# Optimization experiments

Hardware: AMD Instinct MI355X
Metric: run time of the kernel (lower is better)

Reference implementation:

```python
import jax, jax.numpy as jnp
import numpy as np

N = 50000
E = 500000
HID = 64
HEADS = 4
LAYERS = 4
CDIM = 8


def _p(key, shape, scale=0.05):
    return jax.random.normal(key, shape, dtype=jnp.float32) * scale


def setup_inputs() -> dict:
    key = jax.random.key(0)
    ks = jax.random.split(key, 32)
    x = jax.random.normal(ks[0], (N, 8), dtype=jnp.float32)
    src = jax.random.randint(ks[1], (E,), 0, N)
    dst = jax.random.randint(ks[2], (E,), 0, N)
    edge_index = jnp.stack([src, dst]).astype(jnp.int64)
    HC = HEADS * HID
    inp = {
        "x": x,
        "edge_index": edge_index,
        # encoder: Linear(8,64), ELU, Linear(64,64), ELU
        "enc_w1": _p(ks[3], (HID, 8)), "enc_b1": _p(ks[4], (HID,)),
        "enc_w2": _p(ks[5], (HID, HID)), "enc_b2": _p(ks[6], (HID,)),
        # per-layer TransformerConv params, stacked over layers
        "Wq": _p(ks[7], (LAYERS, HC, HID)), "bq": _p(ks[8], (LAYERS, HC)),
        "Wk": _p(ks[9], (LAYERS, HC, HID)), "bk": _p(ks[10], (LAYERS, HC)),
        "Wv": _p(ks[11], (LAYERS, HC, HID)), "bv": _p(ks[12], (LAYERS, HC)),
        "Ws": _p(ks[13], (LAYERS, HID, HID)), "bs": _p(ks[14], (LAYERS, HID)),
        # output MLP: 64->64->32->8
        "out_w1": _p(ks[15], (64, HID)), "out_b1": _p(ks[16], (64,)),
        "out_w2": _p(ks[17], (32, 64)), "out_b2": _p(ks[18], (32,)),
        "out_w3": _p(ks[19], (CDIM, 32)), "out_b3": _p(ks[20], (CDIM,)),
    }
    return inp


def transformer_conv(h, src, dst, Wq, bq, Wk, bk, Wv, bv, Ws, bs):
    """PyG TransformerConv, concat=False, root_weight=True, eval mode (no dropout)."""
    n = h.shape[0]
    q = (h @ Wq.T + bq).reshape(n, HEADS, HID)
    k = (h @ Wk.T + bk).reshape(n, HEADS, HID)
    v = (h @ Wv.T + bv).reshape(n, HEADS, HID)
    # per-edge multi-head scores: (E, H)
    alpha = jnp.einsum("ehd,ehd->eh", q[dst], k[src]) / np.sqrt(HID).astype(np.float32)
    # segment softmax over edges grouped by destination node
    amax = jax.ops.segment_max(alpha, dst, num_segments=n)          # (N, H)
    ex = jnp.exp(alpha - amax[dst])                                 # (E, H)
    denom = jax.ops.segment_sum(ex, dst, num_segments=n)           # (N, H)
    w = ex / denom[dst]                                             # (E, H)
    msg = v[src] * w[:, :, None]                                    # (E, H, C)
    agg = jax.ops.segment_sum(msg, dst, num_segments=n)            # (N, H, C)
    out = agg.mean(axis=1)                                          # concat=False -> head mean
    return out + h @ Ws.T + bs                                      # skip connection


def reference(x, edge_index, enc_w1, enc_b1, enc_w2, enc_b2,
              Wq, bq, Wk, bk, Wv, bv, Ws, bs,
              out_w1, out_b1, out_w2, out_b2, out_w3, out_b3):
    src, dst = edge_index[0], edge_index[1]
    elu = jax.nn.elu
    h = elu(x @ enc_w1.T + enc_b1)
    h = elu(h @ enc_w2.T + enc_b2)
    for l in range(LAYERS):
        h = elu(transformer_conv(h, src, dst, Wq[l], bq[l], Wk[l], bk[l],
                                 Wv[l], bv[l], Ws[l], bs[l]))
        # dropout is identity in eval mode
    o = elu(h @ out_w1.T + out_b1)
    o = elu(o @ out_w2.T + out_b2)
    o = o @ out_w3.T + out_b3
    return o
```

## Files before the change

kernel.cpp:

```cpp
#include <hip/hip_runtime.h>
#include <hip/hip_bf16.h>

#define N_NODES 50000
#define N_EDGES 500000
constexpr int HID = 64;
constexpr int HC  = 256;

typedef unsigned short u16;
typedef unsigned char u8;
typedef __attribute__((ext_vector_type(8))) __bf16 bf16x8;
typedef __attribute__((ext_vector_type(4))) float f32x4;
typedef __attribute__((ext_vector_type(2))) float f32x2;

__device__ __forceinline__ float b2f(u16 u) {
    union { unsigned int i; float f; } c; c.i = ((unsigned int)u) << 16; return c.f;
}
__device__ __forceinline__ u16 f2b(float f) {
    union { float f; unsigned int i; } c; c.f = f;
    unsigned int x = c.i;
    unsigned int lsb = (x >> 16) & 1u;
    x += 0x7fffu + lsb;
    return (u16)(x >> 16);
}
__device__ __forceinline__ float elu_f(float x) { return x > 0.f ? x : expm1f(x); }


__global__ __launch_bounds__(256) void init_kernel(int* __restrict__ cnt, int* __restrict__ cursor) {
    int i = blockIdx.x * 256 + threadIdx.x;
    if (i < N_NODES) { cnt[i] = 0; cursor[i] = 0; }
}

__global__ __launch_bounds__(256) void detect_kernel(const int* __restrict__ ei, int* __restrict__ flag) {
    __shared__ int s[4];
    int t = threadIdx.x;
    int nz = ei[2 * t + 1] != 0;
    unsigned long long m = __ballot(nz);
    if ((t & 63) == 0) s[t >> 6] = (m != 0ull) ? 1 : 0;
    __syncthreads();
    if (t == 0) flag[0] = s[0] | s[1] | s[2] | s[3];
}

__global__ __launch_bounds__(256) void wcvt_kernel(const float* __restrict__ Wq, const float* __restrict__ Wk,
                                                   const float* __restrict__ Wv, const float* __restrict__ Wsk,
                                                   u16* __restrict__ w16) {
    int i = blockIdx.x * 256 + threadIdx.x;
    if (i >= 53248) return;
    const float* src; int off;
    if (i < 16384)      { src = Wq;  off = i; }
    else if (i < 32768) { src = Wk;  off = i - 16384; }
    else if (i < 49152) { src = Wv;  off = i - 32768; }
    else                { src = Wsk; off = i - 49152; }
    float4 v = ((const float4*)src)[off];
    ushort4 u; u.x = f2b(v.x); u.y = f2b(v.y); u.z = f2b(v.z); u.w = f2b(v.w);
    ((ushort4*)w16)[i] = u;
}

__global__ __launch_bounds__(256) void hist_kernel(const int* __restrict__ ei, const int* __restrict__ flag,
                                                   int* __restrict__ cnt) {
    int e = blockIdx.x * 256 + threadIdx.x;
    if (e < N_EDGES) {
        int d = flag[0] ? ei[N_EDGES + e] : ei[2 * N_EDGES + 2 * e];
        atomicAdd(&cnt[d], 1);
    }
}

__global__ __launch_bounds__(512) void scan1_kernel(const int* __restrict__ cnt,
                                                    int* __restrict__ row_start, int* __restrict__ bsum) {
    __shared__ int sc[512];
    int t = threadIdx.x;
    int i = blockIdx.x * 512 + t;
    int v = (i < N_NODES) ? cnt[i] : 0;
    sc[t] = v;
    __syncthreads();
    for (int off = 1; off < 512; off <<= 1) {
        int u = (t >= off) ? sc[t - off] : 0;
        __syncthreads();
        sc[t] += u;
        __syncthreads();
    }
    if (i < N_NODES) row_start[i] = sc[t] - v;
    if (t == 511) bsum[blockIdx.x] = sc[511];
}

__global__ __launch_bounds__(128) void scan2_kernel(int* __restrict__ bsum, int* __restrict__ row_start) {
    __shared__ int sc[128];
    const int NB = (N_NODES + 511) / 512;
    int t = threadIdx.x;
    int v = (t < NB) ? bsum[t] : 0;
    sc[t] = v;
    __syncthreads();
    for (int off = 1; off < 128; off <<= 1) {
        int u = (t >= off) ? sc[t - off] : 0;
        __syncthreads();
        sc[t] += u;
        __syncthreads();
    }
    if (t < NB) bsum[t] = sc[t] - v;
    if (t == 127) row_start[N_NODES] = sc[127];
}

__global__ __launch_bounds__(512) void scan3_kernel(int* __restrict__ row_start, const int* __restrict__ bsum) {
    int i = blockIdx.x * 512 + threadIdx.x;
    if (i < N_NODES) row_start[i] += bsum[blockIdx.x];
}

__global__ __launch_bounds__(256) void scatter_kernel(const int* __restrict__ ei, const int* __restrict__ flag,
                                const int* __restrict__ row_start, int* __restrict__ cursor,
                                int* __restrict__ csr_src) {
    int e = blockIdx.x * 256 + threadIdx.x;
    if (e < N_EDGES) {
        int isI32 = flag[0];
        int s = isI32 ? ei[e] : ei[2 * e];
        int d = isI32 ? ei[N_EDGES + e] : ei[2 * N_EDGES + 2 * e];
        int pos = row_start[d] + atomicAdd(&cursor[d], 1);
        csr_src[pos] = s;
    }
}

__global__ __launch_bounds__(256) void encoder_kernel(const float* __restrict__ x,
                               const float* __restrict__ w1, const float* __restrict__ b1,
                               const float* __restrict__ w2, const float* __restrict__ b2,
                               float* __restrict__ h) {
    __shared__ float xs[64 * 9];
    __shared__ float w1s[64 * 9];
    __shared__ u16 t1s[64 * 72];
    __shared__ u16 w2s[64 * 72];
    __shared__ float b1s[64], b2s[64];
    int t = threadIdx.x;
    int m0 = blockIdx.x * 64;

    if (t < 128) {
        int row = t >> 1, c = (t & 1) * 4;
        float4 val = make_float4(0.f, 0.f, 0.f, 0.f);
        if (m0 + row < N_NODES) val = *(const float4*)(x + (size_t)(m0 + row) * 8 + c);
        *(float4*)&xs[row * 9 + c] = val;
    }
    if (t >= 128 && t < 256) {
        int p = t - 128;
        int row = p >> 1, c = (p & 1) * 4;
        float4 val = *(const float4*)(w1 + row * 8 + c);
        *(float4*)&w1s[row * 9 + c] = val;
    }
    #pragma unroll
    for (int r = 0; r < 4; ++r) {
        int p = t + r * 256; int row = p >> 4, kc = (p & 15) * 4;
        float4 val = *(const float4*)(w2 + row * 64 + kc);
        ushort4 u; u.x = f2b(val.x); u.y = f2b(val.y); u.z = f2b(val.z); u.w = f2b(val.w);
        *(ushort4*)&w2s[row * 72 + kc] = u;
    }
    if (t < 64) { b1s[t] = b1[t]; b2s[t] = b2[t]; }
    __syncthreads();

    {
        int j = t & 63, sub = t >> 6;
        #pragma unroll
        for (int g = 0; g < 16; ++g) {
            int node = g * 4 + sub;
            float acc = b1s[j];
            #pragma unroll
            for (int m = 0; m < 8; ++m) acc += xs[node * 9 + m] * w1s[j * 9 + m];
            t1s[node * 72 + j] = f2b(elu_f(acc));
        }
    }
    __syncthreads();

    int wave = t >> 6, lane = t & 63;
    int lrow = lane & 15, quad = lane >> 4;
    int m_off = wave * 16;
    bf16x8 a0 = *(const bf16x8*)&t1s[(m_off + lrow) * 72 + quad * 8];
    bf16x8 a1 = *(const bf16x8*)&t1s[(m_off + lrow) * 72 + 32 + quad * 8];
    #pragma unroll
    for (int nsub = 0; nsub < 4; ++nsub) {
        bf16x8 b0 = *(const bf16x8*)&w2s[(nsub * 16 + lrow) * 72 + quad * 8];
        bf16x8 b1v = *(const bf16x8*)&w2s[(nsub * 16 + lrow) * 72 + 32 + quad * 8];
        f32x4 acc = {0.f, 0.f, 0.f, 0.f};
        acc = __builtin_amdgcn_mfma_f32_16x16x32_bf16(a0, b0, acc, 0, 0, 0);
        acc = __builtin_amdgcn_mfma_f32_16x16x32_bf16(a1, b1v, acc, 0, 0, 0);
        int col = nsub * 16 + lrow;
        float bias = b2s[col];
        #pragma unroll
        for (int r = 0; r < 4; ++r) {
            int row = m0 + m_off + quad * 4 + r;
            if (row < N_NODES) h[(size_t)row * 64 + col] = elu_f(acc[r] + bias);
        }
    }
}

__global__ __launch_bounds__(256) void proj_kernel(const float* __restrict__ h,
    const u16* __restrict__ wq16, const u16* __restrict__ wk16,
    const u16* __restrict__ wv16, const u16* __restrict__ wsk16,
    const float* __restrict__ bq, const float* __restrict__ bk,
    const float* __restrict__ bv, const float* __restrict__ bsk,
    int layer,
    u16* __restrict__ q, u8* __restrict__ kv, float* __restrict__ skip)
{
    __shared__ u16 as_tile[64 * 72];
    __shared__ u16 ws_tile[64 * 72];
    __shared__ float pool[64 * 68];
    u16* qst  = (u16*)pool;
    u8*  kvst = (u8*)pool;
    float* skst = pool;

    int t = threadIdx.x;
    int m0 = blockIdx.x * 64;

    #pragma unroll
    for (int r = 0; r < 4; ++r) {
        int p = t + r * 256; int row = p >> 4, kc = (p & 15) * 4;
        float4 val = make_float4(0.f, 0.f, 0.f, 0.f);
        if (m0 + row < N_NODES) val = *(const float4*)(h + (size_t)(m0 + row) * 64 + kc);
        ushort4 u; u.x = f2b(val.x); u.y = f2b(val.y); u.z = f2b(val.z); u.w = f2b(val.w);
        *(ushort4*)&as_tile[row * 72 + kc] = u;
    }
    __syncthreads();

    int wave = t >> 6, lane = t & 63;
    int lrow = lane & 15, quad = lane >> 4;
    bf16x8 a0 = *(const bf16x8*)&as_tile[(wave * 16 + lrow) * 72 + quad * 8];
    bf16x8 a1 = *(const bf16x8*)&as_tile[(wave * 16 + lrow) * 72 + 32 + quad * 8];

    const u16* Wq16  = wq16  + (size_t)layer * HC * HID;
    const u16* Wk16  = wk16  + (size_t)layer * HC * HID;
    const u16* Wv16  = wv16  + (size_t)layer * HC * HID;
    const u16* Wsk16 = wsk16 + (size_t)layer * HID * HID;
    const float* bqL  = bq  + layer * HC;
    const float* bkL  = bk  + layer * HC;
    const float* bvL  = bv  + layer * HC;
    const float* bskL = bsk + layer * HID;

    int nl = wave * 16 + lrow;

    auto tile_base = [&](int idx) -> const u16* {
        if (idx < 4) return Wq16 + (size_t)(idx * 64) * 64;
        if (idx < 12) {
            int p2 = idx - 4; int ctk = p2 >> 1;
            return ((p2 & 1) ? Wv16 : Wk16) + (size_t)(ctk * 64) * 64;
        }
        return Wsk16;
    };

    int p0 = t, p1 = t + 256;
    int g_off0 = (p0 >> 3) * 64 + (p0 & 7) * 8;
    int g_off1 = (p1 >> 3) * 64 + (p1 & 7) * 8;
    int l_off0 = (p0 >> 3) * 72 + (p0 & 7) * 8;
    int l_off1 = (p1 >> 3) * 72 + (p1 & 7) * 8;

    uint4 pre0 = *(const uint4*)(tile_base(0) + g_off0);
    uint4 pre1 = *(const uint4*)(tile_base(0) + g_off1);

    for (int idx = 0; idx < 13; ++idx) {
        const float* bt; int cbase; int mode;
        if (idx < 4)       { bt = bqL + idx * 64; cbase = idx * 64; mode = 0; }
        else if (idx < 12) { int p2 = idx - 4; int ctk = p2 >> 1; cbase = ctk * 64;
                             if ((p2 & 1) == 0) { bt = bkL + cbase; mode = 1; }
                             else               { bt = bvL + cbase; mode = 2; } }
        else               { bt = bskL; cbase = 0; mode = 3; }

        __syncthreads();
        *(uint4*)&ws_tile[l_off0] = pre0;
        *(uint4*)&ws_tile[l_off1] = pre1;
        if (idx + 1 < 13) {
            pre0 = *(const uint4*)(tile_base(idx + 1) + g_off0);
            pre1 = *(const uint4*)(tile_base(idx + 1) + g_off1);
        }
        __syncthreads();

        #pragma unroll
        for (int nsub = 0; nsub < 4; ++nsub) {
            bf16x8 w0 = *(const bf16x8*)&ws_tile[(nsub * 16 + lrow) * 72 + quad * 8];
            bf16x8 w1 = *(const bf16x8*)&ws_tile[(nsub * 16 + lrow) * 72 + 32 + quad * 8];
            f32x4 acc = {0.f, 0.f, 0.f, 0.f};
            acc = __builtin_amdgcn_mfma_f32_16x16x32_bf16(w0, a0, acc, 0, 0, 0);
            acc = __builtin_amdgcn_mfma_f32_16x16x32_bf16(w1, a1, acc, 0, 0, 0);
            float4 b4 = *(const float4*)(bt + nsub * 16 + quad * 4);
            if (mode == 0) {
                ushort4 o;
                o.x = f2b(acc[0] + b4.x); o.y = f2b(acc[1] + b4.y);
                o.z = f2b(acc[2] + b4.z); o.w = f2b(acc[3] + b4.w);
                *(ushort4*)&qst[nl * 72 + nsub * 16 + quad * 4] = o;
            } else if (mode == 1 || mode == 2) {
                float f0 = (acc[0] + b4.x) * 16.f, f1 = (acc[1] + b4.y) * 16.f;
                float f2v = (acc[2] + b4.z) * 16.f, f3v = (acc[3] + b4.w) * 16.f;
                int pk = __builtin_amdgcn_cvt_pk_fp8_f32(f0, f1, 0, false);
                pk = __builtin_amdgcn_cvt_pk_fp8_f32(f2v, f3v, pk, true);
                int g = nsub * 4 + quad;
                *(unsigned int*)&kvst[nl * 144 + g * 8 + (mode == 2 ? 4 : 0)] = (unsigned int)pk;
            } else {
                float4 o;
                o.x = acc[0] + b4.x; o.y = acc[1] + b4.y;
                o.z = acc[2] + b4.z; o.w = acc[3] + b4.w;
                *(float4*)&skst[nl * 68 + nsub * 16 + quad * 4] = o;
            }
        }

        if (mode == 0) {
            __syncthreads();
            #pragma unroll
            for (int it = 0; it < 2; ++it) {
                int p = t + it * 256; int row = p >> 3, ch = p & 7;
                int grow = m0 + row;
                if (grow < N_NODES)
                    *(uint4*)(q + (size_t)grow * 256 + cbase + ch * 8) = *(const uint4*)&qst[row * 72 + ch * 8];
            }
        } else if (mode == 2) {
            __syncthreads();
            #pragma unroll
            for (int it = 0; it < 2; ++it) {
                int p = t + it * 256; int row = p >> 3, ch = p & 7;
                int grow = m0 + row;
                if (grow < N_NODES)
                    *(uint4*)(kv + (size_t)grow * 512 + cbase * 2 + ch * 16) = *(const uint4*)&kvst[row * 144 + ch * 16];
            }
        } else if (mode == 3) {
            __syncthreads();
            int row = t >> 2, c0 = (t & 3) * 16;
            int grow = m0 + row;
            if (grow < N_NODES) {
                #pragma unroll
                for (int j = 0; j < 4; ++j)
                    *(float4*)(skip + (size_t)grow * 64 + c0 + j * 4) = *(const float4*)&skst[row * 68 + c0 + j * 4];
            }
        }
    }
}

__global__ __launch_bounds__(256) void attn_kernel(
    const u16* __restrict__ q, const u8* __restrict__ kv,
    const float* __restrict__ skip,
    const int* __restrict__ row_start, const int* __restrict__ csr_src,
    float* __restrict__ hout)
{
    int wave = threadIdx.x >> 6;
    int lane = threadIdx.x & 63;
    int n = blockIdx.x * 4 + wave;
    if (n >= N_NODES) return;
    const float SC = 0.0078125f * 1.44269504f;
    ushort4 q4 = ((const ushort4*)(q + (size_t)n * 256))[lane];
    float qf0 = b2f(q4.x) * SC, qf1 = b2f(q4.y) * SC, qf2 = b2f(q4.z) * SC, qf3 = b2f(q4.w) * SC;
    const u8* kvl = kv + lane * 8;
    float l = 0.f;
    float a0 = 0.f, a1 = 0.f, a2 = 0.f, a3 = 0.f;
    int e0 = __builtin_amdgcn_readfirstlane(row_start[n]);
    int e1 = __builtin_amdgcn_readfirstlane(row_start[n + 1]);
    int elast = (e1 - 1 > e0) ? e1 - 1 : e0;
    for (int e = e0; e < e1; e += 4) {
        int rem = e1 - e;
        int i1 = e + 1 <= elast ? e + 1 : elast;
        int i2 = e + 2 <= elast ? e + 2 : elast;
        int i3 = e + 3 <= elast ? e + 3 : elast;
        int s0 = csr_src[e], s1 = csr_src[i1], s2 = csr_src[i2], s3 = csr_src[i3];
        uint2 c0 = *(const uint2*)(kvl + (size_t)s0 * 512);
        uint2 c1 = *(const uint2*)(kvl + (size_t)s1 * 512);
        uint2 c2 = *(const uint2*)(kvl + (size_t)s2 * 512);
        uint2 c3 = *(const uint2*)(kvl + (size_t)s3 * 512);
        f32x2 k0a = __builtin_amdgcn_cvt_pk_f32_fp8(c0.x, false), k0b = __builtin_amdgcn_cvt_pk_f32_fp8(c0.x, true);
        f32x2 k1a = __builtin_amdgcn_cvt_pk_f32_fp8(c1.x, false), k1b = __builtin_amdgcn_cvt_pk_f32_fp8(c1.x, true);
        f32x2 k2a = __builtin_amdgcn_cvt_pk_f32_fp8(c2.x, false), k2b = __builtin_amdgcn_cvt_pk_f32_fp8(c2.x, true);
        f32x2 k3a = __builtin_amdgcn_cvt_pk_f32_fp8(c3.x, false), k3b = __builtin_amdgcn_cvt_pk_f32_fp8(c3.x, true);
        float p0 = qf0 * k0a.x + qf1 * k0a.y + qf2 * k0b.x + qf3 * k0b.y;
        float p1 = qf0 * k1a.x + qf1 * k1a.y + qf2 * k1b.x + qf3 * k1b.y;
        float p2 = qf0 * k2a.x + qf1 * k2a.y + qf2 * k2b.x + qf3 * k2b.y;
        float p3 = qf0 * k3a.x + qf1 * k3a.y + qf2 * k3b.x + qf3 * k3b.y;
        p0 += __shfl_xor(p0, 1); p1 += __shfl_xor(p1, 1); p2 += __shfl_xor(p2, 1); p3 += __shfl_xor(p3, 1);
        p0 += __shfl_xor(p0, 2); p1 += __shfl_xor(p1, 2); p2 += __shfl_xor(p2, 2); p3 += __shfl_xor(p3, 2);
        p0 += __shfl_xor(p0, 4); p1 += __shfl_xor(p1, 4); p2 += __shfl_xor(p2, 4); p3 += __shfl_xor(p3, 4);
        p0 += __shfl_xor(p0, 8); p1 += __shfl_xor(p1, 8); p2 += __shfl_xor(p2, 8); p3 += __shfl_xor(p3, 8);
        float w0 = exp2f(p0);
        float w1 = rem > 1 ? exp2f(p1) : 0.f;
        float w2 = rem > 2 ? exp2f(p2) : 0.f;
        float w3 = rem > 3 ? exp2f(p3) : 0.f;
        l += (w0 + w1) + (w2 + w3);
        f32x2 v0a = __builtin_amdgcn_cvt_pk_f32_fp8(c0.y, false), v0b = __builtin_amdgcn_cvt_pk_f32_fp8(c0.y, true);
        f32x2 v1a = __builtin_amdgcn_cvt_pk_f32_fp8(c1.y, false), v1b = __builtin_amdgcn_cvt_pk_f32_fp8(c1.y, true);
        f32x2 v2a = __builtin_amdgcn_cvt_pk_f32_fp8(c2.y, false), v2b = __builtin_amdgcn_cvt_pk_f32_fp8(c2.y, true);
        f32x2 v3a = __builtin_amdgcn_cvt_pk_f32_fp8(c3.y, false), v3b = __builtin_amdgcn_cvt_pk_f32_fp8(c3.y, true);
        a0 += w0 * v0a.x + w1 * v1a.x + w2 * v2a.x + w3 * v3a.x;
        a1 += w0 * v0a.y + w1 * v1a.y + w2 * v2a.y + w3 * v3a.y;
        a2 += w0 * v0b.x + w1 * v1b.x + w2 * v2b.x + w3 * v3b.x;
        a3 += w0 * v0b.y + w1 * v1b.y + w2 * v2b.y + w3 * v3b.y;
    }
    float inv = l > 0.f ? 1.f / l : 0.f;
    a0 *= inv; a1 *= inv; a2 *= inv; a3 *= inv;
    a0 += __shfl_xor(a0, 16); a0 += __shfl_xor(a0, 32);
    a1 += __shfl_xor(a1, 16); a1 += __shfl_xor(a1, 32);
    a2 += __shfl_xor(a2, 16); a2 += __shfl_xor(a2, 32);
    a3 += __shfl_xor(a3, 16); a3 += __shfl_xor(a3, 32);
    if ((lane >> 4) == 0) {
        const float OS = 0.015625f;
        float4 sk = ((const float4*)(skip + (size_t)n * 64))[lane];
        float4 o;
        o.x = elu_f(OS * a0 + sk.x);
        o.y = elu_f(OS * a1 + sk.y);
        o.z = elu_f(OS * a2 + sk.z);
        o.w = elu_f(OS * a3 + sk.w);
        ((float4*)(hout + (size_t)n * 64))[lane] = o;
    }
}

__global__ __launch_bounds__(256) void mlp_kernel(const float* __restrict__ h,
    const float* __restrict__ w1, const float* __restrict__ b1,
    const float* __restrict__ w2, const float* __restrict__ b2,
    const float* __restrict__ w3, const float* __restrict__ b3,
    float* __restrict__ out)
{
    __shared__ u16 hs[64 * 72];
    __shared__ u16 w1s[64 * 72];
    __shared__ u16 t1s[64 * 72];
    __shared__ u16 w2s[32 * 72];
    __shared__ float t2s[64 * 33];
    __shared__ float w3s[8 * 33];
    __shared__ float b1s[64], b2s[32], b3s[8];
    int t = threadIdx.x;
    int m0 = blockIdx.x * 64;

    #pragma unroll
    for (int r = 0; r < 4; ++r) {
        int p = t + r * 256; int row = p >> 4, kc = (p & 15) * 4;
        float4 val = make_float4(0.f, 0.f, 0.f, 0.f);
        if (m0 + row < N_NODES) val = *(const float4*)(h + (size_t)(m0 + row) * 64 + kc);
        ushort4 u; u.x = f2b(val.x); u.y = f2b(val.y); u.z = f2b(val.z); u.w = f2b(val.w);
        *(ushort4*)&hs[row * 72 + kc] = u;
    }
    #pragma unroll
    for (int r = 0; r < 4; ++r) {
        int p = t + r * 256; int row = p >> 4, kc = (p & 15) * 4;
        float4 val = *(const float4*)(w1 + row * 64 + kc);
        ushort4 u; u.x = f2b(val.x); u.y = f2b(val.y); u.z = f2b(val.z); u.w = f2b(val.w);
        *(ushort4*)&w1s[row * 72 + kc] = u;
    }
    #pragma unroll
    for (int r = 0; r < 2; ++r) {
        int p = t + r * 256; int row = p >> 4, kc = (p & 15) * 4;
        float4 val = *(const float4*)(w2 + row * 64 + kc);
        ushort4 u; u.x = f2b(val.x); u.y = f2b(val.y); u.z = f2b(val.z); u.w = f2b(val.w);
        *(ushort4*)&w2s[row * 72 + kc] = u;
    }
    if (t < 8 * 32) { int r = t >> 5, c = t & 31; w3s[r * 33 + c] = w3[t]; }
    if (t < 64) b1s[t] = b1[t];
    if (t >= 64 && t < 96) b2s[t - 64] = b2[t - 64];
    if (t >= 96 && t < 104) b3s[t - 96] = b3[t - 96];
    __syncthreads();

    int wave = t >> 6, lane = t & 63;
    int lrow = lane & 15, quad = lane >> 4;
    int m_off = wave * 16;

    {
        bf16x8 a0 = *(const bf16x8*)&hs[(m_off + lrow) * 72 + quad * 8];
        bf16x8 a1 = *(const bf16x8*)&hs[(m_off + lrow) * 72 + 32 + quad * 8];
        #pragma unroll
        for (int nsub = 0; nsub < 4; ++nsub) {
            bf16x8 b0 = *(const bf16x8*)&w1s[(nsub * 16 + lrow) * 72 + quad * 8];
            bf16x8 b1v = *(const bf16x8*)&w1s[(nsub * 16 + lrow) * 72 + 32 + quad * 8];
            f32x4 acc = {0.f, 0.f, 0.f, 0.f};
            acc = __builtin_amdgcn_mfma_f32_16x16x32_bf16(a0, b0, acc, 0, 0, 0);
            acc = __builtin_amdgcn_mfma_f32_16x16x32_bf16(a1, b1v, acc, 0, 0, 0);
            int col = nsub * 16 + lrow;
            float bias = b1s[col];
            #pragma unroll
            for (int r = 0; r < 4; ++r) {
                int row = m_off + quad * 4 + r;
                t1s[row * 72 + col] = f2b(elu_f(acc[r] + bias));
            }
        }
    }
    __syncthreads();

    {
        bf16x8 a0 = *(const bf16x8*)&t1s[(m_off + lrow) * 72 + quad * 8];
        bf16x8 a1 = *(const bf16x8*)&t1s[(m_off + lrow) * 72 + 32 + quad * 8];
        #pragma unroll
        for (int nsub = 0; nsub < 2; ++nsub) {
            bf16x8 b0 = *(const bf16x8*)&w2s[(nsub * 16 + lrow) * 72 + quad * 8];
            bf16x8 b1v = *(const bf16x8*)&w2s[(nsub * 16 + lrow) * 72 + 32 + quad * 8];
            f32x4 acc = {0.f, 0.f, 0.f, 0.f};
            acc = __builtin_amdgcn_mfma_f32_16x16x32_bf16(a0, b0, acc, 0, 0, 0);
            acc = __builtin_amdgcn_mfma_f32_16x16x32_bf16(a1, b1v, acc, 0, 0, 0);
            int col = nsub * 16 + lrow;
            float bias = b2s[col];
            #pragma unroll
            for (int r = 0; r < 4; ++r) {
                int row = m_off + quad * 4 + r;
                t2s[row * 33 + col] = elu_f(acc[r] + bias);
            }
        }
    }
    __syncthreads();

    #pragma unroll
    for (int r = 0; r < 2; ++r) {
        int idx = t + r * 256;
        int node = idx >> 3, j = idx & 7;
        int row = m0 + node;
        if (row < N_NODES) {
            float acc = b3s[j];
            #pragma unroll
            for (int kk = 0; kk < 32; ++kk) acc += t2s[node * 33 + kk] * w3s[j * 33 + kk];
            out[(size_t)row * 8 + j] = acc;
        }
    }
}

extern "C" void kernel_launch(void* const* d_in, const int* in_sizes, int n_in,
                              void* d_out, int out_size, void* d_ws, size_t ws_size,
                              hipStream_t stream) {
    (void)in_sizes; (void)n_in; (void)out_size; (void)ws_size;
    const float* x   = (const float*)d_in[0];
    const int* ei    = (const int*)d_in[1];
    const float* ew1 = (const float*)d_in[2];
    const float* eb1 = (const float*)d_in[3];
    const float* ew2 = (const float*)d_in[4];
    const float* eb2 = (const float*)d_in[5];
    const float* Wq  = (const float*)d_in[6];
    const float* bq  = (const float*)d_in[7];
    const float* Wk  = (const float*)d_in[8];
    const float* bk  = (const float*)d_in[9];
    const float* Wv  = (const float*)d_in[10];
    const float* bv  = (const float*)d_in[11];
    const float* Wsk = (const float*)d_in[12];
    const float* bsk = (const float*)d_in[13];
    const float* ow1 = (const float*)d_in[14];
    const float* ob1 = (const float*)d_in[15];
    const float* ow2 = (const float*)d_in[16];
    const float* ob2 = (const float*)d_in[17];
    const float* ow3 = (const float*)d_in[18];
    const float* ob3 = (const float*)d_in[19];

    char* ws = (char*)d_ws;
    size_t off = 0;
    auto alloc = [&](size_t bytes) -> void* {
        void* p = ws + off;
        off += (bytes + 255) & ~(size_t)255;
        return p;
    };
    float* h0    = (float*)alloc((size_t)N_NODES * 64 * 4);
    float* h1    = (float*)alloc((size_t)N_NODES * 64 * 4);
    u16*   q     = (u16*)  alloc((size_t)N_NODES * 256 * 2);
    u8*    kv    = (u8*)   alloc((size_t)N_NODES * 512);
    float* skp   = (float*)alloc((size_t)N_NODES * 64 * 4);
    u16*   w16   = (u16*)  alloc((size_t)212992 * 2);
    int*   cnt   = (int*)  alloc((size_t)N_NODES * 4);
    int*   cursor= (int*)  alloc((size_t)N_NODES * 4);
    int*   rowst = (int*)  alloc((size_t)(N_NODES + 1) * 4);
    int*   csr   = (int*)  alloc((size_t)N_EDGES * 4);
    int*   bsum  = (int*)  alloc(512);
    int*   flag  = (int*)  alloc(256);

    u16* wq16  = w16;
    u16* wk16  = w16 + 65536;
    u16* wv16  = w16 + 131072;
    u16* wsk16 = w16 + 196608;

    const int NB = (N_NODES + 511) / 512;

    init_kernel<<<(N_NODES + 255) / 256, 256, 0, stream>>>(cnt, cursor);
    detect_kernel<<<1, 256, 0, stream>>>(ei, flag);
    wcvt_kernel<<<208, 256, 0, stream>>>(Wq, Wk, Wv, Wsk, w16);
    hist_kernel<<<(N_EDGES + 255) / 256, 256, 0, stream>>>(ei, flag, cnt);
    scan1_kernel<<<NB, 512, 0, stream>>>(cnt, rowst, bsum);
    scan2_kernel<<<1, 128, 0, stream>>>(bsum, rowst);
    scan3_kernel<<<NB, 512, 0, stream>>>(rowst, bsum);
    scatter_kernel<<<(N_EDGES + 255) / 256, 256, 0, stream>>>(ei, flag, rowst, cursor, csr);

    encoder_kernel<<<(N_NODES + 63) / 64, 256, 0, stream>>>(x, ew1, eb1, ew2, eb2, h0);

    float* hin = h0;
    float* hout = h1;
    for (int l = 0; l < 4; ++l) {
        proj_kernel<<<(N_NODES + 63) / 64, 256, 0, stream>>>(hin, wq16, wk16, wv16, wsk16,
                                                             bq, bk, bv, bsk, l, q, kv, skp);
        attn_kernel<<<(N_NODES + 3) / 4, 256, 0, stream>>>(q, kv, skp, rowst, csr, hout);
        float* tmp = hin; hin = hout; hout = tmp;
    }

    mlp_kernel<<<(N_NODES + 63) / 64, 256, 0, stream>>>(hin, ow1, ob1, ow2, ob2, ow3, ob3, (float*)d_out);
}
```

Measured before the change: 478.7 us.

## Store hidden state and skip in bf16 and process 128 rows per proj block

The hidden activations between layers and the skip projection now live in global memory as bf16 rather than fp32, so the encoder, attention epilogue, projection input and MLP input all move half the bytes and no longer convert on load. The projection kernel also handles 128 nodes per block, with each wave computing two 16-row MFMA tiles per weight tile. This halves the weight-tile loads and syncs per node, and the A tile's shared memory is reused as the output staging buffer. The cost is extra bf16 rounding of the skip term and hidden state, plus fewer, larger blocks for the projection.

```diff
diff --git a/kernel.cpp b/kernel.cpp
--- a/kernel.cpp
+++ b/kernel.cpp
@@ -120,7 +120,7 @@
 __global__ __launch_bounds__(256) void encoder_kernel(const float* __restrict__ x,
                                const float* __restrict__ w1, const float* __restrict__ b1,
                                const float* __restrict__ w2, const float* __restrict__ b2,
-                               float* __restrict__ h) {
+                               u16* __restrict__ h) {
     __shared__ float xs[64 * 9];
     __shared__ float w1s[64 * 9];
     __shared__ u16 t1s[64 * 72];
@@ -181,43 +181,43 @@
         #pragma unroll
         for (int r = 0; r < 4; ++r) {
             int row = m0 + m_off + quad * 4 + r;
-            if (row < N_NODES) h[(size_t)row * 64 + col] = elu_f(acc[r] + bias);
-        }
-    }
-}
-
-__global__ __launch_bounds__(256) void proj_kernel(const float* __restrict__ h,
+            if (row < N_NODES) h[(size_t)row * 64 + col] = f2b(elu_f(acc[r] + bias));
+        }
+    }
+}
+
+__global__ __launch_bounds__(256) void proj_kernel(const u16* __restrict__ h,
     const u16* __restrict__ wq16, const u16* __restrict__ wk16,
     const u16* __restrict__ wv16, const u16* __restrict__ wsk16,
     const float* __restrict__ bq, const float* __restrict__ bk,
     const float* __restrict__ bv, const float* __restrict__ bsk,
     int layer,
-    u16* __restrict__ q, u8* __restrict__ kv, float* __restrict__ skip)
+    u16* __restrict__ q, u8* __restrict__ kv, u16* __restrict__ skip)
 {
-    __shared__ u16 as_tile[64 * 72];
+    __shared__ u16 as_tile[128 * 72];
     __shared__ u16 ws_tile[64 * 72];
-    __shared__ float pool[64 * 68];
-    u16* qst  = (u16*)pool;
-    u8*  kvst = (u8*)pool;
-    float* skst = pool;
+    u16* qst  = as_tile;
+    u8*  kvst = (u8*)as_tile;
+    u16* skst = as_tile;
 
     int t = threadIdx.x;
-    int m0 = blockIdx.x * 64;
+    int m0 = blockIdx.x * 128;
 
     #pragma unroll
     for (int r = 0; r < 4; ++r) {
-        int p = t + r * 256; int row = p >> 4, kc = (p & 15) * 4;
-        float4 val = make_float4(0.f, 0.f, 0.f, 0.f);
-        if (m0 + row < N_NODES) val = *(const float4*)(h + (size_t)(m0 + row) * 64 + kc);
-        ushort4 u; u.x = f2b(val.x); u.y = f2b(val.y); u.z = f2b(val.z); u.w = f2b(val.w);
-        *(ushort4*)&as_tile[row * 72 + kc] = u;
+        int p = t + r * 256; int row = p >> 3, kc = (p & 7) * 8;
+        uint4 val = make_uint4(0u, 0u, 0u, 0u);
+        if (m0 + row < N_NODES) val = *(const uint4*)(h + (size_t)(m0 + row) * 64 + kc);
+        *(uint4*)&as_tile[row * 72 + kc] = val;
     }
     __syncthreads();
 
     int wave = t >> 6, lane = t & 63;
     int lrow = lane & 15, quad = lane >> 4;
-    bf16x8 a0 = *(const bf16x8*)&as_tile[(wave * 16 + lrow) * 72 + quad * 8];
-    bf16x8 a1 = *(const bf16x8*)&as_tile[(wave * 16 + lrow) * 72 + 32 + quad * 8];
+    bf16x8 aA0 = *(const bf16x8*)&as_tile[(wave * 32 + lrow) * 72 + quad * 8];
+    bf16x8 aA1 = *(const bf16x8*)&as_tile[(wave * 32 + lrow) * 72 + 32 + quad * 8];
+    bf16x8 aB0 = *(const bf16x8*)&as_tile[(wave * 32 + 16 + lrow) * 72 + quad * 8];
+    bf16x8 aB1 = *(const bf16x8*)&as_tile[(wave * 32 + 16 + lrow) * 72 + 32 + quad * 8];
 
     const u16* Wq16  = wq16  + (size_t)layer * HC * HID;
     const u16* Wk16  = wk16  + (size_t)layer * HC * HID;
@@ -228,7 +228,8 @@
     const float* bvL  = bv  + layer * HC;
     const float* bskL = bsk + layer * HID;
 
-    int nl = wave * 16 + lrow;
+    int nlA = wave * 32 + lrow;
+    int nlB = nlA + 16;
 
     auto tile_base = [&](int idx) -> const u16* {
         if (idx < 4) return Wq16 + (size_t)(idx * 64) * 64;
@@ -269,34 +270,42 @@
         for (int nsub = 0; nsub < 4; ++nsub) {
             bf16x8 w0 = *(const bf16x8*)&ws_tile[(nsub * 16 + lrow) * 72 + quad * 8];
             bf16x8 w1 = *(const bf16x8*)&ws_tile[(nsub * 16 + lrow) * 72 + 32 + quad * 8];
-            f32x4 acc = {0.f, 0.f, 0.f, 0.f};
-            acc = __builtin_amdgcn_mfma_f32_16x16x32_bf16(w0, a0, acc, 0, 0, 0);
-            acc = __builtin_amdgcn_mfma_f32_16x16x32_bf16(w1, a1, acc, 0, 0, 0);
             float4 b4 = *(const float4*)(bt + nsub * 16 + quad * 4);
-            if (mode == 0) {
-                ushort4 o;
-                o.x = f2b(acc[0] + b4.x); o.y = f2b(acc[1] + b4.y);
-                o.z = f2b(acc[2] + b4.z); o.w = f2b(acc[3] + b4.w);
-                *(ushort4*)&qst[nl * 72 + nsub * 16 + quad * 4] = o;
-            } else if (mode == 1 || mode == 2) {
-                float f0 = (acc[0] + b4.x) * 16.f, f1 = (acc[1] + b4.y) * 16.f;
-                float f2v = (acc[2] + b4.z) * 16.f, f3v = (acc[3] + b4.w) * 16.f;
-                int pk = __builtin_amdgcn_cvt_pk_fp8_f32(f0, f1, 0, false);
-                pk = __builtin_amdgcn_cvt_pk_fp8_f32(f2v, f3v, pk, true);
+            f32x4 accA = {0.f, 0.f, 0.f, 0.f};
+            accA = __builtin_amdgcn_mfma_f32_16x16x32_bf16(w0, aA0, accA, 0, 0, 0);
+            accA = __builtin_amdgcn_mfma_f32_16x16x32_bf16(w1, aA1, accA, 0, 0, 0);
+            f32x4 accB = {0.f, 0.f, 0.f, 0.f};
+            accB = __builtin_amdgcn_mfma_f32_16x16x32_bf16(w0, aB0, accB, 0, 0, 0);
+            accB = __builtin_amdgcn_mfma_f32_16x16x32_bf16(w1, aB1, accB, 0, 0, 0);
+            if (mode == 0 || mode == 3) {
+                ushort4 oA, oB;
+                oA.x = f2b(accA[0] + b4.x); oA.y = f2b(accA[1] + b4.y);
+                oA.z = f2b(accA[2] + b4.z); oA.w = f2b(accA[3] + b4.w);
+                oB.x = f2b(accB[0] + b4.x); oB.y = f2b(accB[1] + b4.y);
+                oB.z = f2b(accB[2] + b4.z); oB.w = f2b(accB[3] + b4.w);
+                u16* st = (mode == 0) ? qst : skst;
+                *(ushort4*)&st[nlA * 72 + nsub * 16 + quad * 4] = oA;
+                *(ushort4*)&st[nlB * 72 + nsub * 16 + quad * 4] = oB;
+            } else {
+                float fA0 = (accA[0] + b4.x) * 16.f, fA1 = (accA[1] + b4.y) * 16.f;
+                float fA2 = (accA[2] + b4.z) * 16.f, fA3 = (accA[3] + b4.w) * 16.f;
+                float fB0 = (accB[0] + b4.x) * 16.f, fB1 = (accB[1] + b4.y) * 16.f;
+                float fB2 = (accB[2] + b4.z) * 16.f, fB3 = (accB[3] + b4.w) * 16.f;
+                int pkA = __builtin_amdgcn_cvt_pk_fp8_f32(fA0, fA1, 0, false);
+                pkA = __builtin_amdgcn_cvt_pk_fp8_f32(fA2, fA3, pkA, true);
+                int pkB = __builtin_amdgcn_cvt_pk_fp8_f32(fB0, fB1, 0, false);
+                pkB = __builtin_amdgcn_cvt_pk_fp8_f32(fB2, fB3, pkB, true);
                 int g = nsub * 4 + quad;
-                *(unsigned int*)&kvst[nl * 144 + g * 8 + (mode == 2 ? 4 : 0)] = (unsigned int)pk;
-            } else {
-                float4 o;
-                o.x = acc[0] + b4.x; o.y = acc[1] + b4.y;
-                o.z = acc[2] + b4.z; o.w = acc[3] + b4.w;
-                *(float4*)&skst[nl * 68 + nsub * 16 + quad * 4] = o;
+                int vo = (mode == 2) ? 4 : 0;
+                *(unsigned int*)&kvst[nlA * 144 + g * 8 + vo] = (unsigned int)pkA;
+                *(unsigned int*)&kvst[nlB * 144 + g * 8 + vo] = (unsigned int)pkB;
             }
         }
 
         if (mode == 0) {
             __syncthreads();
             #pragma unroll
-            for (int it = 0; it < 2; ++it) {
+            for (int it = 0; it < 4; ++it) {
                 int p = t + it * 256; int row = p >> 3, ch = p & 7;
                 int grow = m0 + row;
                 if (grow < N_NODES)
@@ -305,7 +314,7 @@
         } else if (mode == 2) {
             __syncthreads();
             #pragma unroll
-            for (int it = 0; it < 2; ++it) {
+            for (int it = 0; it < 4; ++it) {
                 int p = t + it * 256; int row = p >> 3, ch = p & 7;
                 int grow = m0 + row;
                 if (grow < N_NODES)
@@ -313,12 +322,12 @@
             }
         } else if (mode == 3) {
             __syncthreads();
-            int row = t >> 2, c0 = (t & 3) * 16;
-            int grow = m0 + row;
-            if (grow < N_NODES) {
-                #pragma unroll
-                for (int j = 0; j < 4; ++j)
-                    *(float4*)(skip + (size_t)grow * 64 + c0 + j * 4) = *(const float4*)&skst[row * 68 + c0 + j * 4];
+            #pragma unroll
+            for (int it = 0; it < 4; ++it) {
+                int p = t + it * 256; int row = p >> 3, ch = p & 7;
+                int grow = m0 + row;
+                if (grow < N_NODES)
+                    *(uint4*)(skip + (size_t)grow * 64 + ch * 8) = *(const uint4*)&skst[row * 72 + ch * 8];
             }
         }
     }
@@ -326,9 +335,9 @@
 
 __global__ __launch_bounds__(256) void attn_kernel(
     const u16* __restrict__ q, const u8* __restrict__ kv,
-    const float* __restrict__ skip,
+    const u16* __restrict__ skip,
     const int* __restrict__ row_start, const int* __restrict__ csr_src,
-    float* __restrict__ hout)
+    u16* __restrict__ hout)
 {
     int wave = threadIdx.x >> 6;
     int lane = threadIdx.x & 63;
@@ -387,17 +396,17 @@
     a3 += __shfl_xor(a3, 16); a3 += __shfl_xor(a3, 32);
     if ((lane >> 4) == 0) {
         const float OS = 0.015625f;
-        float4 sk = ((const float4*)(skip + (size_t)n * 64))[lane];
-        float4 o;
-        o.x = elu_f(OS * a0 + sk.x);
-        o.y = elu_f(OS * a1 + sk.y);
-        o.z = elu_f(OS * a2 + sk.z);
-        o.w = elu_f(OS * a3 + sk.w);
-        ((float4*)(hout + (size_t)n * 64))[lane] = o;
-    }
-}
-
-__global__ __launch_bounds__(256) void mlp_kernel(const float* __restrict__ h,
+        ushort4 sk4 = *(const ushort4*)(skip + (size_t)n * 64 + lane * 4);
+        ushort4 ov;
+        ov.x = f2b(elu_f(OS * a0 + b2f(sk4.x)));
+        ov.y = f2b(elu_f(OS * a1 + b2f(sk4.y)));
+        ov.z = f2b(elu_f(OS * a2 + b2f(sk4.z)));
+        ov.w = f2b(elu_f(OS * a3 + b2f(sk4.w)));
+        *(ushort4*)(hout + (size_t)n * 64 + lane * 4) = ov;
+    }
+}
+
+__global__ __launch_bounds__(256) void mlp_kernel(const u16* __restrict__ h,
     const float* __restrict__ w1, const float* __restrict__ b1,
     const float* __restrict__ w2, const float* __restrict__ b2,
     const float* __restrict__ w3, const float* __restrict__ b3,
@@ -414,12 +423,11 @@
     int m0 = blockIdx.x * 64;
 
     #pragma unroll
-    for (int r = 0; r < 4; ++r) {
-        int p = t + r * 256; int row = p >> 4, kc = (p & 15) * 4;
-        float4 val = make_float4(0.f, 0.f, 0.f, 0.f);
-        if (m0 + row < N_NODES) val = *(const float4*)(h + (size_t)(m0 + row) * 64 + kc);
-        ushort4 u; u.x = f2b(val.x); u.y = f2b(val.y); u.z = f2b(val.z); u.w = f2b(val.w);
-        *(ushort4*)&hs[row * 72 + kc] = u;
+    for (int r = 0; r < 2; ++r) {
+        int p = t + r * 256; int row = p >> 3, kc = (p & 7) * 8;
+        uint4 val = make_uint4(0u, 0u, 0u, 0u);
+        if (m0 + row < N_NODES) val = *(const uint4*)(h + (size_t)(m0 + row) * 64 + kc);
+        *(uint4*)&hs[row * 72 + kc] = val;
     }
     #pragma unroll
     for (int r = 0; r < 4; ++r) {
@@ -533,11 +541,11 @@
         off += (bytes + 255) & ~(size_t)255;
         return p;
     };
-    float* h0    = (float*)alloc((size_t)N_NODES * 64 * 4);
-    float* h1    = (float*)alloc((size_t)N_NODES * 64 * 4);
+    u16*   h0    = (u16*)  alloc((size_t)N_NODES * 64 * 2);
+    u16*   h1    = (u16*)  alloc((size_t)N_NODES * 64 * 2);
     u16*   q     = (u16*)  alloc((size_t)N_NODES * 256 * 2);
     u8*    kv    = (u8*)   alloc((size_t)N_NODES * 512);
-    float* skp   = (float*)alloc((size_t)N_NODES * 64 * 4);
+    u16*   skp   = (u16*)  alloc((size_t)N_NODES * 64 * 2);
     u16*   w16   = (u16*)  alloc((size_t)212992 * 2);
     int*   cnt   = (int*)  alloc((size_t)N_NODES * 4);
     int*   cursor= (int*)  alloc((size_t)N_NODES * 4);
@@ -564,13 +572,13 @@
 
     encoder_kernel<<<(N_NODES + 63) / 64, 256, 0, stream>>>(x, ew1, eb1, ew2, eb2, h0);
 
-    float* hin = h0;
-    float* hout = h1;
+    u16* hin = h0;
+    u16* hout = h1;
     for (int l = 0; l < 4; ++l) {
-        proj_kernel<<<(N_NODES + 63) / 64, 256, 0, stream>>>(hin, wq16, wk16, wv16, wsk16,
-                                                             bq, bk, bv, bsk, l, q, kv, skp);
+        proj_kernel<<<(N_NODES + 127) / 128, 256, 0, stream>>>(hin, wq16, wk16, wv16, wsk16,
+                                                               bq, bk, bv, bsk, l, q, kv, skp);
         attn_kernel<<<(N_NODES + 3) / 4, 256, 0, stream>>>(q, kv, skp, rowst, csr, hout);
-        float* tmp = hin; hin = hout; hout = tmp;
+        u16* tmp = hin; hin = hout; hout = tmp;
     }
 
     mlp_kernel<<<(N_NODES + 63) / 64, 256, 0, stream>>>(hin, ow1, ob1, ow2, ob2, ow3, ob3, (float*)d_out);
```

Measured after the change: 486.6 us. Within noise of the previous version (+1.7%).
